# Kernel optimization log

Hardware: AMD Instinct MI355X
Metric: run time of the kernel (lower is better)

Reference implementation:

```python
import jax, jax.numpy as jnp
import numpy as np

N = 20000          # nodes
E = 200000         # edges
IN = 256           # in_channels
OUT = 256          # out_channels (heads * per-head)
H = 2              # heads
C = OUT // 2       # per-head channels (out_channels // 2)
TDIM = 100         # time_enc.out_channels
MSG = 156          # msg_dim
EDGE_DIM = TDIM + MSG  # 256
P = 0.1            # dropout prob


def setup_inputs() -> dict:
    key = jax.random.key(0)
    ks = jax.random.split(key, 20)
    s = 1.0 / np.sqrt(IN)
    se = 1.0 / np.sqrt(EDGE_DIM)
    return {
        "x": jax.random.normal(ks[0], (N, IN), jnp.float32),
        "last_update": jax.random.uniform(ks[1], (N,), jnp.float32) * 100.0,
        "edge_index": jax.random.randint(ks[2], (2, E), 0, N, jnp.int64),
        "t": jax.random.uniform(ks[3], (E,), jnp.float32) * 100.0,
        "msg": jax.random.normal(ks[4], (E, MSG), jnp.float32),
        "u_edge": jax.random.uniform(ks[5], (E,), jnp.float32),
        "u_attn": jax.random.uniform(ks[6], (E, H), jnp.float32),
        # TimeEncoder: cos(Linear(1, TDIM))
        "time_w": jax.random.normal(ks[7], (TDIM,), jnp.float32),
        "time_b": jax.random.normal(ks[8], (TDIM,), jnp.float32) * 0.1,
        # TransformerConv params ([in, out] layout)
        "Wq": jax.random.normal(ks[9], (IN, H * C), jnp.float32) * s,
        "bq": jnp.zeros((H * C,), jnp.float32),
        "Wk": jax.random.normal(ks[10], (IN, H * C), jnp.float32) * s,
        "bk": jnp.zeros((H * C,), jnp.float32),
        "Wv": jax.random.normal(ks[11], (IN, H * C), jnp.float32) * s,
        "bv": jnp.zeros((H * C,), jnp.float32),
        "We": jax.random.normal(ks[12], (EDGE_DIM, H * C), jnp.float32) * se,
        "be": jnp.zeros((H * C,), jnp.float32),
        "Ws": jax.random.normal(ks[13], (IN, H * C), jnp.float32) * s,
        "bs": jnp.zeros((H * C,), jnp.float32),
    }


def reference(x, last_update, edge_index, t, msg, u_edge, u_attn,
              time_w, time_b, Wq, bq, Wk, bk, Wv, bv, We, be, Ws, bs):
    src, dst = edge_index[0], edge_index[1]
    # time encoding of relative time (TGN TimeEncoder: cos(Linear(1, TDIM)))
    rel_t = last_update[src] - t                              # [E]
    rel_enc = jnp.cos(rel_t[:, None] * time_w[None, :] + time_b)  # [E, TDIM]
    edge_attr = jnp.concatenate([rel_enc, msg], axis=-1)      # [E, EDGE_DIM]
    # dropout_adj: drop edges with prob P (no rescale)
    keep = u_edge > P                                         # [E] bool

    q = (x @ Wq + bq).reshape(N, H, C)
    k = (x @ Wk + bk).reshape(N, H, C)
    v = (x @ Wv + bv).reshape(N, H, C)
    e = (edge_attr @ We + be).reshape(E, H, C)

    kj = k[src] + e                                           # [E, H, C]
    alpha = jnp.einsum('ehc,ehc->eh', q[dst], kj) / jnp.sqrt(jnp.float32(C))
    alpha = jnp.where(keep[:, None], alpha, -jnp.inf)
    # segment softmax over incoming edges of each dst node
    m = jax.ops.segment_max(alpha, dst, num_segments=N)       # [N, H]
    m = jnp.where(jnp.isfinite(m), m, 0.0)
    ex = jnp.where(keep[:, None], jnp.exp(alpha - m[dst]), 0.0)
    denom = jax.ops.segment_sum(ex, dst, num_segments=N)      # [N, H]
    attn = ex / (denom[dst] + 1e-16)                          # [E, H]
    # attention dropout (post-softmax, inverted scaling)
    attn = attn * (u_attn > P).astype(attn.dtype) / (1.0 - P)

    msg_out = (v[src] + e) * attn[:, :, None]                 # [E, H, C]
    out = jax.ops.segment_sum(msg_out, dst, num_segments=N).reshape(N, H * C)
    # root/skip connection
    return out + (x @ Ws + bs)
```

## Files before the change

### kernel.cpp

```cpp
#include <hip/hip_runtime.h>

#define NND 20000
#define NE 200000
#define PDROP 0.1f

typedef unsigned short u16;
typedef __bf16 bf16x8 __attribute__((ext_vector_type(8)));
typedef float f32x4 __attribute__((ext_vector_type(4)));

__device__ __forceinline__ float b2f(u16 u) {
  unsigned v = ((unsigned)u) << 16;
  float f;
  __builtin_memcpy(&f, &v, 4);
  return f;
}
__device__ __forceinline__ u16 f2b(float f) {
  unsigned x;
  __builtin_memcpy(&x, &f, 4);
  unsigned r = x + 0x7fffu + ((x >> 16) & 1u);
  return (u16)(r >> 16);
}

__global__ void convert_x(const float* __restrict__ x, u16* __restrict__ xb) {
  int i = blockIdx.x * blockDim.x + threadIdx.x;
  if (i < NND * 256 / 4) {
    float4 v = ((const float4*)x)[i];
    ushort4 o;
    o.x = f2b(v.x); o.y = f2b(v.y); o.z = f2b(v.z); o.w = f2b(v.w);
    ((ushort4*)xb)[i] = o;
  }
}

struct WTArgs {
  const float* W[6];
  u16* WT[6];
};
__global__ void convert_wT(WTArgs a) {
  int gid = blockIdx.x * blockDim.x + threadIdx.x;
  if (gid >= 6 * 65536) return;
  int w = gid >> 16, r = gid & 65535;
  if (w < 5) {
    int n = r >> 8, k = r & 255;
    a.WT[w][n * 256 + k] = f2b(a.W[w][k * 256 + n]);
  } else {
    a.WT[5][r] = f2b(a.W[5][r]);
  }
}

__global__ void zero2(int* __restrict__ cnt, int* __restrict__ cur) {
  int i = blockIdx.x * blockDim.x + threadIdx.x;
  if (i < NND) { cnt[i] = 0; cur[i] = 0; }
}
__global__ void csr_count(const int* __restrict__ ei, int* __restrict__ cnt) {
  int e = blockIdx.x * blockDim.x + threadIdx.x;
  if (e < NE) atomicAdd(&cnt[ei[NE + e]], 1);
}
__global__ __launch_bounds__(1024) void scan_rowptr(const int* __restrict__ cnt,
                                                    int* __restrict__ rowptr) {
  __shared__ int sums[1024];
  const int tid = threadIdx.x;
  const int base = tid * 20;
  int local[20];
  int run = 0;
#pragma unroll
  for (int i = 0; i < 20; i++) {
    int idx = base + i;
    local[i] = run;
    run += (idx < NND) ? cnt[idx] : 0;
  }
  sums[tid] = run;
  __syncthreads();
  for (int off = 1; off < 1024; off <<= 1) {
    int v = (tid >= off) ? sums[tid - off] : 0;
    __syncthreads();
    sums[tid] += v;
    __syncthreads();
  }
  int prev = (tid > 0) ? sums[tid - 1] : 0;
#pragma unroll
  for (int i = 0; i < 20; i++) {
    int idx = base + i;
    if (idx < NND) rowptr[idx] = prev + local[i];
  }
  if (tid == 1023) rowptr[NND] = sums[1023];
}
__global__ void csr_fill(const int* __restrict__ ei, const int* __restrict__ rowptr,
                         int* __restrict__ cur, int* __restrict__ elist) {
  int e = blockIdx.x * blockDim.x + threadIdx.x;
  if (e < NE) {
    int d = ei[NE + e];
    int p = rowptr[d] + atomicAdd(&cur[d], 1);
    elist[p] = e;
  }
}

__device__ __forceinline__ void mfma_tile(const u16 (*As)[72], const u16 (*Bs)[72],
                                          f32x4 acc[4][4], int wm, int wn,
                                          int fr, int fg) {
#pragma unroll
  for (int ks = 0; ks < 2; ks++) {
    bf16x8 a[4], b[4];
#pragma unroll
    for (int i = 0; i < 4; i++)
      a[i] = *(const bf16x8*)&As[wm * 64 + i * 16 + fr][ks * 32 + fg * 8];
#pragma unroll
    for (int j = 0; j < 4; j++)
      b[j] = *(const bf16x8*)&Bs[wn * 64 + j * 16 + fr][ks * 32 + fg * 8];
#pragma unroll
    for (int i = 0; i < 4; i++)
#pragma unroll
      for (int j = 0; j < 4; j++)
        acc[i][j] = __builtin_amdgcn_mfma_f32_16x16x32_bf16(a[i], b[j], acc[i][j], 0, 0, 0);
  }
}

struct NodeArgs {
  const u16* BT[4];
  const float* bias[4];
  u16* outb[3];
  float* outf;
};
__global__ __launch_bounds__(256) void gemm_node(const u16* __restrict__ xb,
                                                 NodeArgs args) {
  __shared__ __attribute__((aligned(16))) u16 As[128][72];
  __shared__ __attribute__((aligned(16))) u16 Bs[128][72];
  const int tid = threadIdx.x;
  const int w = blockIdx.y >> 1;
  const int col0 = (blockIdx.y & 1) * 128;
  const int row0 = blockIdx.x * 128;
  const u16* BT = args.BT[w];
  const float* bias = args.bias[w];
  const int wid = tid >> 6, lane = tid & 63;
  const int wm = wid >> 1, wn = wid & 1;
  const int fr = lane & 15, fg = lane >> 4;
  f32x4 acc[4][4] = {};
  for (int k0 = 0; k0 < 256; k0 += 64) {
#pragma unroll
    for (int i = 0; i < 4; i++) {
      int idx = tid + i * 256;
      int row = idx >> 3, vc = idx & 7;
      int g = row0 + row;
      uint4 v = make_uint4(0, 0, 0, 0);
      if (g < NND) v = *(const uint4*)&xb[(size_t)g * 256 + k0 + vc * 8];
      *(uint4*)&As[row][vc * 8] = v;
      *(uint4*)&Bs[row][vc * 8] = *(const uint4*)&BT[(size_t)(col0 + row) * 256 + k0 + vc * 8];
    }
    __syncthreads();
    mfma_tile(As, Bs, acc, wm, wn, fr, fg);
    __syncthreads();
  }
#pragma unroll
  for (int mi = 0; mi < 4; mi++) {
#pragma unroll
    for (int rr = 0; rr < 4; rr++) {
      int grow = row0 + wm * 64 + mi * 16 + fg * 4 + rr;
      if (grow >= NND) continue;
#pragma unroll
      for (int ni = 0; ni < 4; ni++) {
        int gcol = col0 + wn * 64 + ni * 16 + fr;
        float val = acc[mi][ni][rr] + bias[gcol];
        if (w < 3)
          args.outb[w][(size_t)grow * 256 + gcol] = f2b(val);
        else
          args.outf[(size_t)grow * 256 + gcol] = val;
      }
    }
  }
}

__global__ __launch_bounds__(256) void gemm_qwe(const u16* __restrict__ qb,
                                                const u16* __restrict__ Web,
                                                u16* __restrict__ qWeb) {
  __shared__ __attribute__((aligned(16))) u16 As[128][72];
  __shared__ __attribute__((aligned(16))) u16 Bs[128][72];
  const int tid = threadIdx.x;
  const int h = blockIdx.y >> 1;
  const int col0 = (blockIdx.y & 1) * 128;
  const int row0 = blockIdx.x * 128;
  const int wid = tid >> 6, lane = tid & 63;
  const int wm = wid >> 1, wn = wid & 1;
  const int fr = lane & 15, fg = lane >> 4;
  f32x4 acc[4][4] = {};
  for (int k0 = 0; k0 < 128; k0 += 64) {
#pragma unroll
    for (int i = 0; i < 4; i++) {
      int idx = tid + i * 256;
      int row = idx >> 3, vc = idx & 7;
      int g = row0 + row;
      uint4 v = make_uint4(0, 0, 0, 0);
      if (g < NND) v = *(const uint4*)&qb[(size_t)g * 256 + h * 128 + k0 + vc * 8];
      *(uint4*)&As[row][vc * 8] = v;
      *(uint4*)&Bs[row][vc * 8] =
          *(const uint4*)&Web[(size_t)(col0 + row) * 256 + h * 128 + k0 + vc * 8];
    }
    __syncthreads();
    mfma_tile(As, Bs, acc, wm, wn, fr, fg);
    __syncthreads();
  }
#pragma unroll
  for (int mi = 0; mi < 4; mi++) {
#pragma unroll
    for (int rr = 0; rr < 4; rr++) {
      int grow = row0 + wm * 64 + mi * 16 + fg * 4 + rr;
      if (grow >= NND) continue;
#pragma unroll
      for (int ni = 0; ni < 4; ni++) {
        int gj = col0 + wn * 64 + ni * 16 + fr;
        qWeb[(size_t)grow * 512 + h * 256 + gj] = f2b(acc[mi][ni][rr]);
      }
    }
  }
}

__global__ __launch_bounds__(256) void node_fused(
    const u16* __restrict__ qb, const u16* __restrict__ kb,
    const u16* __restrict__ vb, const u16* __restrict__ qWeb,
    const int* __restrict__ ei, const float* __restrict__ last_update,
    const float* __restrict__ t, const float* __restrict__ msg,
    const float* __restrict__ tw, const float* __restrict__ tb_,
    const float* __restrict__ be, const float* __restrict__ u_edge,
    const float* __restrict__ u_attn, const int* __restrict__ rowptr,
    const int* __restrict__ elist, u16* __restrict__ aggb,
    float* __restrict__ out) {
  const int node = (blockIdx.x * blockDim.x + threadIdx.x) >> 6;
  const int lane = threadIdx.x & 63;
  if (node >= NND) return;
  const int beg = rowptr[node], end = rowptr[node + 1];
  const int c0 = lane * 4, hl = lane >> 5;

  ushort4 q4 = *(const ushort4*)&qb[(size_t)node * 256 + c0];
  float qf0 = b2f(q4.x), qf1 = b2f(q4.y), qf2 = b2f(q4.z), qf3 = b2f(q4.w);
  ushort4 w0v = *(const ushort4*)&qWeb[(size_t)node * 512 + c0];
  ushort4 w1v = *(const ushort4*)&qWeb[(size_t)node * 512 + 256 + c0];
  float qw00 = b2f(w0v.x), qw01 = b2f(w0v.y), qw02 = b2f(w0v.z), qw03 = b2f(w0v.w);
  float qw10 = b2f(w1v.x), qw11 = b2f(w1v.y), qw12 = b2f(w1v.z), qw13 = b2f(w1v.w);
  float4 bev = *(const float4*)&be[c0];
  float pb = qf0 * bev.x + qf1 * bev.y + qf2 * bev.z + qf3 * bev.w;
#pragma unroll
  for (int off = 16; off; off >>= 1) pb += __shfl_xor(pb, off);
  float tw0 = 0, tw1 = 0, tw2 = 0, tw3 = 0, tb0 = 0, tb1 = 0, tb2 = 0, tb3 = 0;
  if (c0 < 100) {
    float4 a = *(const float4*)&tw[c0];
    float4 b = *(const float4*)&tb_[c0];
    tw0 = a.x; tw1 = a.y; tw2 = a.z; tw3 = a.w;
    tb0 = b.x; tb1 = b.y; tb2 = b.z; tb3 = b.w;
  }
  const float inv = 0.08838834764831845f;

  float m0 = -INFINITY, m1 = -INFINITY;
  float den0 = 0.f, den1 = 0.f, sw0 = 0.f, sw1 = 0.f;
  float vc0 = 0, vc1 = 0, vc2 = 0, vc3 = 0;
  float g00 = 0, g01 = 0, g02 = 0, g03 = 0;
  float g10 = 0, g11 = 0, g12 = 0, g13 = 0;

  for (int j = beg; j < end; ++j) {
    int eid = elist[j];
    int s = ei[eid];
    float rt = last_update[s] - t[eid];
    ushort4 k4 = *(const ushort4*)&kb[(size_t)s * 256 + c0];
    ushort4 v4 = *(const ushort4*)&vb[(size_t)s * 256 + c0];
    bool keep = u_edge[eid] > PDROP;
    float2 ua = *(const float2*)&u_attn[(size_t)eid * 2];
    float ea0, ea1, ea2, ea3;
    if (c0 < 100) {
      ea0 = __cosf(rt * tw0 + tb0); ea1 = __cosf(rt * tw1 + tb1);
      ea2 = __cosf(rt * tw2 + tb2); ea3 = __cosf(rt * tw3 + tb3);
    } else {
      float4 mm = *(const float4*)&msg[(size_t)eid * 156 + (c0 - 100)];
      ea0 = mm.x; ea1 = mm.y; ea2 = mm.z; ea3 = mm.w;
    }
    float pqk = qf0 * b2f(k4.x) + qf1 * b2f(k4.y) + qf2 * b2f(k4.z) + qf3 * b2f(k4.w);
    float pe0 = qw00 * ea0 + qw01 * ea1 + qw02 * ea2 + qw03 * ea3;
    float pe1 = qw10 * ea0 + qw11 * ea1 + qw12 * ea2 + qw13 * ea3;
    float y0 = pe0 + __shfl_xor(pe0, 32);
    float y1 = pe1 + __shfl_xor(pe1, 32);
    float z = (lane < 32) ? y0 : y1;
#pragma unroll
    for (int off = 16; off; off >>= 1) {
      z += __shfl_xor(z, off);
      pqk += __shfl_xor(pqk, off);
    }
    float a = keep ? (pqk + z + pb) * inv : -INFINITY;
    float aoth = __shfl_xor(a, 32);
    float a0 = (lane < 32) ? a : aoth;
    float a1 = (lane < 32) ? aoth : a;
    if (a0 > m0) {
      float sc = (m0 > -1e30f) ? __expf(m0 - a0) : 0.f;
      den0 *= sc; sw0 *= sc;
      g00 *= sc; g01 *= sc; g02 *= sc; g03 *= sc;
      float scv = hl ? 1.f : sc;
      vc0 *= scv; vc1 *= scv; vc2 *= scv; vc3 *= scv;
      m0 = a0;
    }
    if (a1 > m1) {
      float sc = (m1 > -1e30f) ? __expf(m1 - a1) : 0.f;
      den1 *= sc; sw1 *= sc;
      g10 *= sc; g11 *= sc; g12 *= sc; g13 *= sc;
      float scv = hl ? sc : 1.f;
      vc0 *= scv; vc1 *= scv; vc2 *= scv; vc3 *= scv;
      m1 = a1;
    }
    float ex0 = (a0 > -1e30f) ? __expf(a0 - m0) : 0.f;
    float ex1 = (a1 > -1e30f) ? __expf(a1 - m1) : 0.f;
    den0 += ex0; den1 += ex1;
    float w0 = ex0 * ((ua.x > PDROP) ? (1.f / 0.9f) : 0.f);
    float w1 = ex1 * ((ua.y > PDROP) ? (1.f / 0.9f) : 0.f);
    float wv = hl ? w1 : w0;
    vc0 += wv * b2f(v4.x); vc1 += wv * b2f(v4.y);
    vc2 += wv * b2f(v4.z); vc3 += wv * b2f(v4.w);
    g00 += w0 * ea0; g01 += w0 * ea1; g02 += w0 * ea2; g03 += w0 * ea3;
    g10 += w1 * ea0; g11 += w1 * ea1; g12 += w1 * ea2; g13 += w1 * ea3;
    sw0 += w0; sw1 += w1;
  }

  float rden0 = 1.f / (den0 + 1e-16f), rden1 = 1.f / (den1 + 1e-16f);
  float rv = hl ? rden1 : rden0;
  float swv = hl ? sw1 : sw0;
  float4 o = *(float4*)&out[(size_t)node * 256 + c0];
  o.x += (vc0 + swv * bev.x) * rv;
  o.y += (vc1 + swv * bev.y) * rv;
  o.z += (vc2 + swv * bev.z) * rv;
  o.w += (vc3 + swv * bev.w) * rv;
  *(float4*)&out[(size_t)node * 256 + c0] = o;
  ushort4 a0v, a1v;
  a0v.x = f2b(g00 * rden0); a0v.y = f2b(g01 * rden0);
  a0v.z = f2b(g02 * rden0); a0v.w = f2b(g03 * rden0);
  a1v.x = f2b(g10 * rden1); a1v.y = f2b(g11 * rden1);
  a1v.z = f2b(g12 * rden1); a1v.w = f2b(g13 * rden1);
  *(ushort4*)&aggb[(size_t)node * 256 + c0] = a0v;
  *(ushort4*)&aggb[(size_t)(NND + node) * 256 + c0] = a1v;
}

__global__ __launch_bounds__(256) void gemm_final(const u16* __restrict__ aggb,
                                                  const u16* __restrict__ WeT,
                                                  float* __restrict__ out) {
  __shared__ __attribute__((aligned(16))) u16 As[128][72];
  __shared__ __attribute__((aligned(16))) u16 Bs[128][72];
  const int tid = threadIdx.x;
  const int h = blockIdx.y;
  const int row0 = blockIdx.x * 128;
  const u16* A = aggb + (size_t)h * NND * 256;
  const int wid = tid >> 6, lane = tid & 63;
  const int wm = wid >> 1, wn = wid & 1;
  const int fr = lane & 15, fg = lane >> 4;
  f32x4 acc[4][4] = {};
  for (int k0 = 0; k0 < 256; k0 += 64) {
#pragma unroll
    for (int i = 0; i < 4; i++) {
      int idx = tid + i * 256;
      int row = idx >> 3, vc = idx & 7;
      int g = row0 + row;
      uint4 v = make_uint4(0, 0, 0, 0);
      if (g < NND) v = *(const uint4*)&A[(size_t)g * 256 + k0 + vc * 8];
      *(uint4*)&As[row][vc * 8] = v;
      *(uint4*)&Bs[row][vc * 8] =
          *(const uint4*)&WeT[(size_t)(h * 128 + row) * 256 + k0 + vc * 8];
    }
    __syncthreads();
    mfma_tile(As, Bs, acc, wm, wn, fr, fg);
    __syncthreads();
  }
#pragma unroll
  for (int mi = 0; mi < 4; mi++) {
#pragma unroll
    for (int rr = 0; rr < 4; rr++) {
      int grow = row0 + wm * 64 + mi * 16 + fg * 4 + rr;
      if (grow >= NND) continue;
#pragma unroll
      for (int ni = 0; ni < 4; ni++) {
        int gcol = wn * 64 + ni * 16 + fr;
        out[(size_t)grow * 256 + h * 128 + gcol] += acc[mi][ni][rr];
      }
    }
  }
}

extern "C" void kernel_launch(void* const* d_in, const int* in_sizes, int n_in,
                              void* d_out, int out_size, void* d_ws, size_t ws_size,
                              hipStream_t stream) {
  const float* x = (const float*)d_in[0];
  const float* last_update = (const float*)d_in[1];
  const int* ei = (const int*)d_in[2];
  const float* t = (const float*)d_in[3];
  const float* msg = (const float*)d_in[4];
  const float* u_edge = (const float*)d_in[5];
  const float* u_attn = (const float*)d_in[6];
  const float* time_w = (const float*)d_in[7];
  const float* time_b = (const float*)d_in[8];
  const float* Wq = (const float*)d_in[9];
  const float* bq = (const float*)d_in[10];
  const float* Wk = (const float*)d_in[11];
  const float* bk = (const float*)d_in[12];
  const float* Wv = (const float*)d_in[13];
  const float* bv = (const float*)d_in[14];
  const float* We = (const float*)d_in[15];
  const float* be = (const float*)d_in[16];
  const float* Ws = (const float*)d_in[17];
  const float* bs = (const float*)d_in[18];
  float* out = (float*)d_out;

  char* ws = (char*)d_ws;
  u16* xb = (u16*)(ws + 0);
  u16* WT0 = (u16*)(ws + 10240000);
  u16* qb = (u16*)(ws + 11026432);
  u16* kb = (u16*)(ws + 21266432);
  u16* vb = (u16*)(ws + 31506432);
  u16* qWeb = (u16*)(ws + 41746432);
  u16* aggb = (u16*)(ws + 62226432);
  int* cnt = (int*)(ws + 82706432);
  int* cur = (int*)(ws + 82786432);
  int* rowptr = (int*)(ws + 82866432);
  int* elist = (int*)(ws + 82946448);

  zero2<<<(NND + 255) / 256, 256, 0, stream>>>(cnt, cur);
  csr_count<<<(NE + 255) / 256, 256, 0, stream>>>(ei, cnt);
  scan_rowptr<<<1, 1024, 0, stream>>>(cnt, rowptr);
  csr_fill<<<(NE + 255) / 256, 256, 0, stream>>>(ei, rowptr, cur, elist);

  WTArgs wa;
  wa.W[0] = Wq; wa.W[1] = Wk; wa.W[2] = Wv; wa.W[3] = Ws; wa.W[4] = We; wa.W[5] = We;
  for (int i = 0; i < 6; i++) wa.WT[i] = WT0 + (size_t)i * 65536;
  convert_wT<<<(6 * 65536 + 255) / 256, 256, 0, stream>>>(wa);
  convert_x<<<(NND * 64 + 255) / 256, 256, 0, stream>>>(x, xb);

  NodeArgs na;
  na.BT[0] = wa.WT[0]; na.BT[1] = wa.WT[1]; na.BT[2] = wa.WT[2]; na.BT[3] = wa.WT[3];
  na.bias[0] = bq; na.bias[1] = bk; na.bias[2] = bv; na.bias[3] = bs;
  na.outb[0] = qb; na.outb[1] = kb; na.outb[2] = vb;
  na.outf = out;
  dim3 gn((NND + 127) / 128, 8);
  gemm_node<<<gn, 256, 0, stream>>>(xb, na);

  dim3 gq((NND + 127) / 128, 4);
  gemm_qwe<<<gq, 256, 0, stream>>>(qb, wa.WT[5], qWeb);

  node_fused<<<(NND + 3) / 4, 256, 0, stream>>>(
      qb, kb, vb, qWeb, ei, last_update, t, msg, time_w, time_b, be, u_edge,
      u_attn, rowptr, elist, aggb, out);

  dim3 gf((NND + 127) / 128, 2);
  gemm_final<<<gf, 256, 0, stream>>>(aggb, wa.WT[4], out);
}
```

Baseline: 238.4 us.

## Pack per-edge records in CSR order and prefetch next edge in node kernel

```diff
diff --git a/kernel.cpp b/kernel.cpp
--- a/kernel.cpp
+++ b/kernel.cpp
@@ -84,13 +84,28 @@
   }
   if (tid == 1023) rowptr[NND] = sums[1023];
 }
-__global__ void csr_fill(const int* __restrict__ ei, const int* __restrict__ rowptr,
-                         int* __restrict__ cur, int* __restrict__ elist) {
+__global__ void csr_fill(const int* __restrict__ ei,
+                         const float* __restrict__ last_update,
+                         const float* __restrict__ t,
+                         const float* __restrict__ u_edge,
+                         const float* __restrict__ u_attn,
+                         const int* __restrict__ rowptr, int* __restrict__ cur,
+                         int* __restrict__ elist, uint4* __restrict__ recs) {
   int e = blockIdx.x * blockDim.x + threadIdx.x;
   if (e < NE) {
+    int s = ei[e];
     int d = ei[NE + e];
     int p = rowptr[d] + atomicAdd(&cur[d], 1);
     elist[p] = e;
+    bool keep = u_edge[e] > PDROP;
+    float rt = last_update[s] - t[e];
+    float2 ua = *(const float2*)&u_attn[(size_t)e * 2];
+    uint4 r;
+    r.x = (unsigned)s | (keep ? 0u : 0x80000000u);
+    r.y = __float_as_uint(rt);
+    r.z = __float_as_uint(ua.x > PDROP ? (1.f / 0.9f) : 0.f);
+    r.w = __float_as_uint(ua.y > PDROP ? (1.f / 0.9f) : 0.f);
+    recs[p] = r;
   }
 }
 
@@ -215,12 +230,10 @@
 __global__ __launch_bounds__(256) void node_fused(
     const u16* __restrict__ qb, const u16* __restrict__ kb,
     const u16* __restrict__ vb, const u16* __restrict__ qWeb,
-    const int* __restrict__ ei, const float* __restrict__ last_update,
-    const float* __restrict__ t, const float* __restrict__ msg,
-    const float* __restrict__ tw, const float* __restrict__ tb_,
-    const float* __restrict__ be, const float* __restrict__ u_edge,
-    const float* __restrict__ u_attn, const int* __restrict__ rowptr,
-    const int* __restrict__ elist, u16* __restrict__ aggb,
+    const float* __restrict__ msg, const float* __restrict__ tw,
+    const float* __restrict__ tb_, const float* __restrict__ be,
+    const int* __restrict__ rowptr, const int* __restrict__ elist,
+    const uint4* __restrict__ recs, u16* __restrict__ aggb,
     float* __restrict__ out) {
   const int node = (blockIdx.x * blockDim.x + threadIdx.x) >> 6;
   const int lane = threadIdx.x & 63;
@@ -253,23 +266,41 @@
   float g00 = 0, g01 = 0, g02 = 0, g03 = 0;
   float g10 = 0, g11 = 0, g12 = 0, g13 = 0;
 
+  unsigned seC = 0; float rtC = 0, wk0C = 0, wk1C = 0;
+  ushort4 k4C = make_ushort4(0, 0, 0, 0), v4C = make_ushort4(0, 0, 0, 0);
+  float4 mmC = make_float4(0, 0, 0, 0);
+
+#define LOAD_SLOT(J, se, rt, w0_, w1_, k4, v4, mm)                        \
+  {                                                                       \
+    uint4 rr_ = recs[J];                                                  \
+    se = rr_.x; rt = __uint_as_float(rr_.y);                              \
+    w0_ = __uint_as_float(rr_.z); w1_ = __uint_as_float(rr_.w);           \
+    int s_ = (int)(se & 0x7fffffffu);                                     \
+    k4 = *(const ushort4*)&kb[(size_t)s_ * 256 + c0];                     \
+    v4 = *(const ushort4*)&vb[(size_t)s_ * 256 + c0];                     \
+    if (c0 >= 100) {                                                      \
+      int eid_ = elist[J];                                                \
+      mm = *(const float4*)&msg[(size_t)eid_ * 156 + (c0 - 100)];         \
+    }                                                                     \
+  }
+
+  if (beg < end) LOAD_SLOT(beg, seC, rtC, wk0C, wk1C, k4C, v4C, mmC);
+
   for (int j = beg; j < end; ++j) {
-    int eid = elist[j];
-    int s = ei[eid];
-    float rt = last_update[s] - t[eid];
-    ushort4 k4 = *(const ushort4*)&kb[(size_t)s * 256 + c0];
-    ushort4 v4 = *(const ushort4*)&vb[(size_t)s * 256 + c0];
-    bool keep = u_edge[eid] > PDROP;
-    float2 ua = *(const float2*)&u_attn[(size_t)eid * 2];
+    unsigned seN = 0; float rtN = 0, wk0N = 0, wk1N = 0;
+    ushort4 k4N = make_ushort4(0, 0, 0, 0), v4N = make_ushort4(0, 0, 0, 0);
+    float4 mmN = make_float4(0, 0, 0, 0);
+    if (j + 1 < end) LOAD_SLOT(j + 1, seN, rtN, wk0N, wk1N, k4N, v4N, mmN);
+
     float ea0, ea1, ea2, ea3;
     if (c0 < 100) {
-      ea0 = __cosf(rt * tw0 + tb0); ea1 = __cosf(rt * tw1 + tb1);
-      ea2 = __cosf(rt * tw2 + tb2); ea3 = __cosf(rt * tw3 + tb3);
+      ea0 = __cosf(rtC * tw0 + tb0); ea1 = __cosf(rtC * tw1 + tb1);
+      ea2 = __cosf(rtC * tw2 + tb2); ea3 = __cosf(rtC * tw3 + tb3);
     } else {
-      float4 mm = *(const float4*)&msg[(size_t)eid * 156 + (c0 - 100)];
-      ea0 = mm.x; ea1 = mm.y; ea2 = mm.z; ea3 = mm.w;
-    }
-    float pqk = qf0 * b2f(k4.x) + qf1 * b2f(k4.y) + qf2 * b2f(k4.z) + qf3 * b2f(k4.w);
+      ea0 = mmC.x; ea1 = mmC.y; ea2 = mmC.z; ea3 = mmC.w;
+    }
+    float pqk = qf0 * b2f(k4C.x) + qf1 * b2f(k4C.y) +
+                qf2 * b2f(k4C.z) + qf3 * b2f(k4C.w);
     float pe0 = qw00 * ea0 + qw01 * ea1 + qw02 * ea2 + qw03 * ea3;
     float pe1 = qw10 * ea0 + qw11 * ea1 + qw12 * ea2 + qw13 * ea3;
     float y0 = pe0 + __shfl_xor(pe0, 32);
@@ -280,7 +311,7 @@
       z += __shfl_xor(z, off);
       pqk += __shfl_xor(pqk, off);
     }
-    float a = keep ? (pqk + z + pb) * inv : -INFINITY;
+    float a = (seC < 0x80000000u) ? (pqk + z + pb) * inv : -INFINITY;
     float aoth = __shfl_xor(a, 32);
     float a0 = (lane < 32) ? a : aoth;
     float a1 = (lane < 32) ? aoth : a;
@@ -303,15 +334,19 @@
     float ex0 = (a0 > -1e30f) ? __expf(a0 - m0) : 0.f;
     float ex1 = (a1 > -1e30f) ? __expf(a1 - m1) : 0.f;
     den0 += ex0; den1 += ex1;
-    float w0 = ex0 * ((ua.x > PDROP) ? (1.f / 0.9f) : 0.f);
-    float w1 = ex1 * ((ua.y > PDROP) ? (1.f / 0.9f) : 0.f);
+    float w0 = ex0 * wk0C;
+    float w1 = ex1 * wk1C;
     float wv = hl ? w1 : w0;
-    vc0 += wv * b2f(v4.x); vc1 += wv * b2f(v4.y);
-    vc2 += wv * b2f(v4.z); vc3 += wv * b2f(v4.w);
+    vc0 += wv * b2f(v4C.x); vc1 += wv * b2f(v4C.y);
+    vc2 += wv * b2f(v4C.z); vc3 += wv * b2f(v4C.w);
     g00 += w0 * ea0; g01 += w0 * ea1; g02 += w0 * ea2; g03 += w0 * ea3;
     g10 += w1 * ea0; g11 += w1 * ea1; g12 += w1 * ea2; g13 += w1 * ea3;
     sw0 += w0; sw1 += w1;
-  }
+
+    seC = seN; rtC = rtN; wk0C = wk0N; wk1C = wk1N;
+    k4C = k4N; v4C = v4N; mmC = mmN;
+  }
+#undef LOAD_SLOT
 
   float rden0 = 1.f / (den0 + 1e-16f), rden1 = 1.f / (den1 + 1e-16f);
   float rv = hl ? rden1 : rden0;
@@ -407,15 +442,18 @@
   u16* vb = (u16*)(ws + 31506432);
   u16* qWeb = (u16*)(ws + 41746432);
   u16* aggb = (u16*)(ws + 62226432);
-  int* cnt = (int*)(ws + 82706432);
-  int* cur = (int*)(ws + 82786432);
-  int* rowptr = (int*)(ws + 82866432);
-  int* elist = (int*)(ws + 82946448);
+  uint4* recs = (uint4*)(ws + 82706432);
+  int* cnt = (int*)(ws + 85906432);
+  int* cur = (int*)(ws + 85986432);
+  int* rowptr = (int*)(ws + 86066432);
+  int* elist = (int*)(ws + 86146448);
 
   zero2<<<(NND + 255) / 256, 256, 0, stream>>>(cnt, cur);
   csr_count<<<(NE + 255) / 256, 256, 0, stream>>>(ei, cnt);
   scan_rowptr<<<1, 1024, 0, stream>>>(cnt, rowptr);
-  csr_fill<<<(NE + 255) / 256, 256, 0, stream>>>(ei, rowptr, cur, elist);
+  csr_fill<<<(NE + 255) / 256, 256, 0, stream>>>(ei, last_update, t, u_edge,
+                                                 u_attn, rowptr, cur, elist,
+                                                 recs);
 
   WTArgs wa;
   wa.W[0] = Wq; wa.W[1] = Wk; wa.W[2] = Wv; wa.W[3] = Ws; wa.W[4] = We; wa.W[5] = We;
@@ -435,8 +473,8 @@
   gemm_qwe<<<gq, 256, 0, stream>>>(qb, wa.WT[5], qWeb);
 
   node_fused<<<(NND + 3) / 4, 256, 0, stream>>>(
-      qb, kb, vb, qWeb, ei, last_update, t, msg, time_w, time_b, be, u_edge,
-      u_attn, rowptr, elist, aggb, out);
+      qb, kb, vb, qWeb, msg, time_w, time_b, be, rowptr, elist, recs, aggb,
+      out);
 
   dim3 gf((NND + 127) / 128, 2);
   gemm_final<<<gf, 256, 0, stream>>>(aggb, wa.WT[4], out);
```

Result: slower. 264.4 us (+10.9%).
